# Kernel tuning notes

Measured on AMD Instinct MI355X. Metric: run time of the kernel, lower is better.

## Reference

```python
import jax, jax.numpy as jnp
import numpy as np

B, N, D, H = 8, 128, 768, 64
NEG = -1e30
SLOPE = 0.01  # LeakyReLU slope
EPS = 1e-5    # BatchNorm eps


def setup_inputs() -> dict:
    key = jax.random.key(0)
    ks = jax.random.split(key, 10)
    s = 0.02
    feature = jax.random.normal(ks[0], (B, N, D), jnp.float32)
    aspect = jax.random.normal(ks[1], (B, D), jnp.float32)
    adj = jax.random.randint(ks[2], (B, N, N), 0, 2).astype(jnp.int32)
    W0 = jax.random.normal(ks[3], (D, D), jnp.float32) * s
    b0 = jnp.zeros((D,), jnp.float32)
    W1 = jax.random.normal(ks[4], (D, D), jnp.float32) * s
    b1 = jnp.zeros((D,), jnp.float32)
    A1 = jax.random.normal(ks[5], (2 * D, H), jnp.float32) * s  # afcs[0]
    ab1 = jnp.zeros((H,), jnp.float32)
    A2 = jax.random.normal(ks[6], (H, 1), jnp.float32) * s      # afcs[2]
    ab2 = jnp.zeros((1,), jnp.float32)
    gamma = jnp.ones((D,), jnp.float32)
    beta = jnp.zeros((D,), jnp.float32)
    return dict(feature=feature, aspect=aspect, adj=adj, W0=W0, b0=b0,
                W1=W1, b1=b1, A1=A1, ab1=ab1, A2=A2, ab2=ab2,
                gamma=gamma, beta=beta)


def reference(feature, aspect, adj, W0, b0, W1, b1, A1, ab1, A2, ab2, gamma, beta):
    # aspect is unused by the original forward.
    m = adj.astype(feature.dtype)          # [B,N,N] 0/1 mask
    d = A1.shape[0] // 2
    A1s, A1t = A1[:d], A1[d:]              # weight-split of Linear(2*mem_dim, H):
                                           # [h_i, h_j] @ A1 == h_i @ A1s + h_j @ A1t
    for (W, b) in ((W0, b0), (W1, b1)):
        h = feature @ W + b                # [B,N,D]
        s_src = h @ A1s                    # [B,N,H], broadcast over j
        s_tgt = h @ A1t                    # [B,N,H], broadcast over i
        hid = jax.nn.relu(s_src[:, :, None, :] + s_tgt[:, None, :, :] + ab1)  # [B,N,N,H]
        e = (hid @ A2)[..., 0] + ab2[0]    # [B,N,N]
        e = jnp.where(e > 0, e, SLOPE * e)  # LeakyReLU(0.01)
        logits = e * m + (1.0 - m) * NEG    # mask_logits
        b_, n_ = logits.shape[0], logits.shape[1]
        # NOTE: original softmaxes over the FLATTENED N*N axis, not per-row.
        attn = jax.nn.softmax(logits.reshape(b_, n_ * n_), axis=-1).reshape(b_, n_, n_)
        feature = jnp.einsum('bij,bjd->bid', attn, h)  # attention.bmm(h)
        # dropout is identity in eval / deterministic reference
    node_feature = feature
    g = node_feature.sum(axis=1)           # [B,D]
    mean = g.mean(axis=0)
    var = g.var(axis=0)                    # biased, matches BN training forward
    graph_feature = gamma * (g - mean) / jnp.sqrt(var + EPS) + beta
    return graph_feature, node_feature
```

## Files before the change

kernel.cpp:

```cpp
#include <hip/hip_runtime.h>
#include <math.h>

#define NEG_V (-1e30f)
#define SLOPE_V 0.01f
#define EPS_V 1e-5f

typedef __attribute__((ext_vector_type(8))) short bs8;
typedef __attribute__((ext_vector_type(4))) float f32x4;

__device__ __forceinline__ void split2(float x, unsigned short& hi, unsigned short& lo) {
    unsigned u = __float_as_uint(x);
    unsigned h = (u + 0x7FFFu + ((u >> 16) & 1u)) >> 16;
    hi = (unsigned short)h;
    float hf = __uint_as_float(h << 16);
    float l = x - hf;
    unsigned ul = __float_as_uint(l);
    lo = (unsigned short)((ul + 0x7FFFu + ((ul >> 16) & 1u)) >> 16);
}

__device__ __forceinline__ void mfma_loop(
    const unsigned short* __restrict__ Ahg, const unsigned short* __restrict__ Alg,
    int lda,
    const unsigned short* __restrict__ Bhg, const unsigned short* __restrict__ Blg,
    int ldb, int K, int row0, int col0,
    f32x4 (&acc)[2][2],
    unsigned short (*buf)[64][40])
{
    const int tid = threadIdx.x;
    const int lane = tid & 63, wid = tid >> 6;
    const int wm0 = (wid >> 1) * 32, wn0 = (wid & 1) * 32;
    const int lm = lane & 15, q = lane >> 4;
    const int sr = tid >> 2, sc = (tid & 3) * 8;

    const unsigned short* pAh = Ahg + (size_t)(row0 + sr) * lda + sc;
    const unsigned short* pAl = Alg + (size_t)(row0 + sr) * lda + sc;
    const unsigned short* pBh = Bhg + (size_t)(col0 + sr) * ldb + sc;
    const unsigned short* pBl = Blg + (size_t)(col0 + sr) * ldb + sc;

    bs8 rAh = *(const bs8*)(pAh);
    bs8 rAl = *(const bs8*)(pAl);
    bs8 rBh = *(const bs8*)(pBh);
    bs8 rBl = *(const bs8*)(pBl);

    int st = 0;
    for (int k0 = 0; k0 < K; k0 += 32) {
        unsigned short (*Ah)[40] = buf[st * 4 + 0];
        unsigned short (*Al)[40] = buf[st * 4 + 1];
        unsigned short (*Bh)[40] = buf[st * 4 + 2];
        unsigned short (*Bl)[40] = buf[st * 4 + 3];
        *(bs8*)&Ah[sr][sc] = rAh;
        *(bs8*)&Al[sr][sc] = rAl;
        *(bs8*)&Bh[sr][sc] = rBh;
        *(bs8*)&Bl[sr][sc] = rBl;
        __syncthreads();
        if (k0 + 32 < K) {
            rAh = *(const bs8*)(pAh + k0 + 32);
            rAl = *(const bs8*)(pAl + k0 + 32);
            rBh = *(const bs8*)(pBh + k0 + 32);
            rBl = *(const bs8*)(pBl + k0 + 32);
        }
        bs8 a_h[2], a_l[2], b_h[2], b_l[2];
#pragma unroll
        for (int t = 0; t < 2; t++) {
            a_h[t] = *(bs8*)&Ah[wm0 + t * 16 + lm][q * 8];
            a_l[t] = *(bs8*)&Al[wm0 + t * 16 + lm][q * 8];
            b_h[t] = *(bs8*)&Bh[wn0 + t * 16 + lm][q * 8];
            b_l[t] = *(bs8*)&Bl[wn0 + t * 16 + lm][q * 8];
        }
#pragma unroll
        for (int mt = 0; mt < 2; mt++)
#pragma unroll
            for (int nt = 0; nt < 2; nt++) {
                acc[mt][nt] = __builtin_amdgcn_mfma_f32_16x16x32_bf16(a_h[mt], b_h[nt], acc[mt][nt], 0, 0, 0);
                acc[mt][nt] = __builtin_amdgcn_mfma_f32_16x16x32_bf16(a_h[mt], b_l[nt], acc[mt][nt], 0, 0, 0);
                acc[mt][nt] = __builtin_amdgcn_mfma_f32_16x16x32_bf16(a_l[mt], b_h[nt], acc[mt][nt], 0, 0, 0);
            }
        st ^= 1;
    }
}

__device__ __forceinline__ void transpose_split_tile(
    const float* __restrict__ src, int src_ld,
    unsigned short* __restrict__ dh, unsigned short* __restrict__ dl, int dst_ld,
    unsigned short (*Th)[72], unsigned short (*Tl)[72])
{
    int tid = threadIdx.x;
    int r = tid >> 2;
    int cb = (tid & 3) * 16;
#pragma unroll
    for (int cc = 0; cc < 16; cc += 4) {
        float4 v = *(const float4*)(src + (size_t)r * src_ld + cb + cc);
        unsigned short hh, ll;
        split2(v.x, hh, ll); Th[cb + cc + 0][r] = hh; Tl[cb + cc + 0][r] = ll;
        split2(v.y, hh, ll); Th[cb + cc + 1][r] = hh; Tl[cb + cc + 1][r] = ll;
        split2(v.z, hh, ll); Th[cb + cc + 2][r] = hh; Tl[cb + cc + 2][r] = ll;
        split2(v.w, hh, ll); Th[cb + cc + 3][r] = hh; Tl[cb + cc + 3][r] = ll;
    }
    __syncthreads();
    int n = tid >> 2, ch = (tid & 3) * 8;
    *(bs8*)(dh + (size_t)n * dst_ld + ch)      = *(bs8*)&Th[n][ch];
    *(bs8*)(dh + (size_t)n * dst_ld + ch + 32) = *(bs8*)&Th[n][ch + 32];
    *(bs8*)(dl + (size_t)n * dst_ld + ch)      = *(bs8*)&Tl[n][ch];
    *(bs8*)(dl + (size_t)n * dst_ld + ch + 32) = *(bs8*)&Tl[n][ch + 32];
}

__device__ __forceinline__ void flat_split_job(
    const float* __restrict__ src, unsigned short* __restrict__ dh,
    unsigned short* __restrict__ dl, size_t base)
{
    unsigned short hh, ll;
#pragma unroll
    for (int g = 0; g < 2; g++) {
        bs8 sh, sl;
#pragma unroll
        for (int cc = 0; cc < 8; cc += 4) {
            float4 v = *(const float4*)(src + base + g * 8 + cc);
            split2(v.x, hh, ll); sh[cc + 0] = (short)hh; sl[cc + 0] = (short)ll;
            split2(v.y, hh, ll); sh[cc + 1] = (short)hh; sl[cc + 1] = (short)ll;
            split2(v.z, hh, ll); sh[cc + 2] = (short)hh; sl[cc + 2] = (short)ll;
            split2(v.w, hh, ll); sh[cc + 3] = (short)hh; sl[cc + 3] = (short)ll;
        }
        *(bs8*)(dh + base + g * 8) = sh;
        *(bs8*)(dl + base + g * 8) = sl;
    }
}

__global__ __launch_bounds__(256) void prep_k(
    const float* __restrict__ W0, const float* __restrict__ W1,
    const float* __restrict__ A1, const float* __restrict__ feature,
    const float* __restrict__ b0, const float* __restrict__ b1,
    unsigned short* Wt0h, unsigned short* Wt0l,
    unsigned short* Wt1h, unsigned short* Wt1l,
    unsigned short* fh, unsigned short* fl,
    unsigned short* WAth, unsigned short* WAtl,
    float* bA)
{
    __shared__ __align__(16) char smem[20480];
    int id = blockIdx.x, tid = threadIdx.x;
    if (id < 288) {
        unsigned short (*Th)[72] = (unsigned short(*)[72])(smem);
        unsigned short (*Tl)[72] = (unsigned short(*)[72])(smem + 9216);
        if (id < 144) {
            int kt = id / 12, nt = id % 12;
            transpose_split_tile(W0 + (size_t)(kt * 64) * 768 + nt * 64, 768,
                                 Wt0h + (size_t)(nt * 64) * 768 + kt * 64,
                                 Wt0l + (size_t)(nt * 64) * 768 + kt * 64, 768, Th, Tl);
        } else {
            int r = id - 144, kt = r / 12, nt = r % 12;
            transpose_split_tile(W1 + (size_t)(kt * 64) * 768 + nt * 64, 768,
                                 Wt1h + (size_t)(nt * 64) * 768 + kt * 64,
                                 Wt1l + (size_t)(nt * 64) * 768 + kt * 64, 768, Th, Tl);
        }
    } else if (id < 480) {
        flat_split_job(feature, fh, fl, (size_t)(id - 288) * 4096 + tid * 16);
    } else if (id < 528) {
        int j = id - 480;
        int rt = j % 12, ct = (j / 12) & 1, layer = j / 24;
        const float* W = layer ? W1 : W0;
        const int r0 = rt * 64;
        unsigned short (*Ah)[40] = (unsigned short(*)[40])(smem);
        unsigned short (*Al)[40] = (unsigned short(*)[40])(smem + 5120);
        unsigned short (*Bh)[40] = (unsigned short(*)[40])(smem + 10240);
        unsigned short (*Bl)[40] = (unsigned short(*)[40])(smem + 15360);
        const int lane = tid & 63, wid = tid >> 6;
        const int wm0 = (wid >> 1) * 32, wn0 = (wid & 1) * 32;
        const int lm = lane & 15, q = lane >> 4;
        const int akk = tid & 31, acs = (tid >> 5) * 8;
        const int br = tid >> 2, bks = (tid & 3) * 8;
        f32x4 acc[2][2] = {};
        for (int k0 = 0; k0 < 768; k0 += 32) {
            {
                const float* ap = A1 + (size_t)(ct * 768 + k0 + akk) * 64 + acs;
                float4 v0 = *(const float4*)ap;
                float4 v1 = *(const float4*)(ap + 4);
                unsigned short hv, lv;
                split2(v0.x, hv, lv); Ah[acs + 0][akk] = hv; Al[acs + 0][akk] = lv;
                split2(v0.y, hv, lv); Ah[acs + 1][akk] = hv; Al[acs + 1][akk] = lv;
                split2(v0.z, hv, lv); Ah[acs + 2][akk] = hv; Al[acs + 2][akk] = lv;
                split2(v0.w, hv, lv); Ah[acs + 3][akk] = hv; Al[acs + 3][akk] = lv;
                split2(v1.x, hv, lv); Ah[acs + 4][akk] = hv; Al[acs + 4][akk] = lv;
                split2(v1.y, hv, lv); Ah[acs + 5][akk] = hv; Al[acs + 5][akk] = lv;
                split2(v1.z, hv, lv); Ah[acs + 6][akk] = hv; Al[acs + 6][akk] = lv;
                split2(v1.w, hv, lv); Ah[acs + 7][akk] = hv; Al[acs + 7][akk] = lv;
            }
            {
                const float* wp = W + (size_t)(r0 + br) * 768 + k0 + bks;
                float4 v0 = *(const float4*)wp;
                float4 v1 = *(const float4*)(wp + 4);
                bs8 sh, sl; unsigned short hv, lv;
                split2(v0.x, hv, lv); sh[0] = (short)hv; sl[0] = (short)lv;
                split2(v0.y, hv, lv); sh[1] = (short)hv; sl[1] = (short)lv;
                split2(v0.z, hv, lv); sh[2] = (short)hv; sl[2] = (short)lv;
                split2(v0.w, hv, lv); sh[3] = (short)hv; sl[3] = (short)lv;
                split2(v1.x, hv, lv); sh[4] = (short)hv; sl[4] = (short)lv;
                split2(v1.y, hv, lv); sh[5] = (short)hv; sl[5] = (short)lv;
                split2(v1.z, hv, lv); sh[6] = (short)hv; sl[6] = (short)lv;
                split2(v1.w, hv, lv); sh[7] = (short)hv; sl[7] = (short)lv;
                *(bs8*)&Bh[br][bks] = sh;
                *(bs8*)&Bl[br][bks] = sl;
            }
            __syncthreads();
            bs8 a_h[2], a_l[2], b_h[2], b_l[2];
#pragma unroll
            for (int t = 0; t < 2; t++) {
                a_h[t] = *(bs8*)&Ah[wm0 + t * 16 + lm][q * 8];
                a_l[t] = *(bs8*)&Al[wm0 + t * 16 + lm][q * 8];
                b_h[t] = *(bs8*)&Bh[wn0 + t * 16 + lm][q * 8];
                b_l[t] = *(bs8*)&Bl[wn0 + t * 16 + lm][q * 8];
            }
#pragma unroll
            for (int mt = 0; mt < 2; mt++)
#pragma unroll
                for (int nt = 0; nt < 2; nt++) {
                    acc[mt][nt] = __builtin_amdgcn_mfma_f32_16x16x32_bf16(a_h[mt], b_h[nt], acc[mt][nt], 0, 0, 0);
                    acc[mt][nt] = __builtin_amdgcn_mfma_f32_16x16x32_bf16(a_h[mt], b_l[nt], acc[mt][nt], 0, 0, 0);
                    acc[mt][nt] = __builtin_amdgcn_mfma_f32_16x16x32_bf16(a_l[mt], b_h[nt], acc[mt][nt], 0, 0, 0);
                }
            __syncthreads();
        }
        const int c0 = ct * 64;
        size_t base = (size_t)layer * 98304;
#pragma unroll
        for (int mt = 0; mt < 2; mt++)
#pragma unroll
            for (int nt = 0; nt < 2; nt++) {
                int n = r0 + wn0 + nt * 16 + lm;
#pragma unroll
                for (int i = 0; i < 4; i++) {
                    int m = c0 + wm0 + mt * 16 + q * 4 + i;
                    unsigned short hv, lv;
                    split2(acc[mt][nt][i], hv, lv);
                    WAth[base + (size_t)m * 768 + n] = hv;
                    WAtl[base + (size_t)m * 768 + n] = lv;
                }
            }
    } else {
        float* redb = (float*)(smem);
        int layer = id - 528;
        const float* bv = layer ? b1 : b0;
        int c = tid & 127, half = tid >> 7;
        float acc = 0.f;
        for (int kk = 0; kk < 384; kk++) {
            int k = half * 384 + kk;
            int row = (c < 64 ? k : 768 + k);
            acc += bv[k] * A1[(size_t)row * 64 + (c & 63)];
        }
        redb[tid] = acc;
        __syncthreads();
        if (tid < 128) bA[layer * 128 + tid] = redb[tid] + redb[tid + 128];
    }
}

__global__ __launch_bounds__(256) void gemm_fused_k(
    const unsigned short* __restrict__ Ahg, const unsigned short* __restrict__ Alg,
    const unsigned short* __restrict__ Wth, const unsigned short* __restrict__ Wtl,
    const unsigned short* __restrict__ WAth, const unsigned short* __restrict__ WAtl,
    const float* __restrict__ bias,
    unsigned short* __restrict__ hth, unsigned short* __restrict__ htl,
    float* __restrict__ s)
{
    __shared__ unsigned short smem[8][64][40];
    int bx = blockIdx.x, row0 = blockIdx.y * 64;
    const unsigned short* Bh;
    const unsigned short* Bl;
    int col0;
    if (bx < 12) { Bh = Wth;  Bl = Wtl;  col0 = bx * 64; }
    else         { Bh = WAth; Bl = WAtl; col0 = (bx - 12) * 64; }
    f32x4 acc[2][2] = {};
    mfma_loop(Ahg, Alg, 768, Bh, Bl, 768, 768, row0, col0, acc, smem);
    int tid = threadIdx.x, lane = tid & 63, wid = tid >> 6;
    int wm0 = (wid >> 1) * 32, wn0 = (wid & 1) * 32;
    int lm = lane & 15, q = lane >> 4;
    if (bx >= 12) {
#pragma unroll
        for (int mt = 0; mt < 2; mt++)
#pragma unroll
            for (int nt = 0; nt < 2; nt++) {
                int c = col0 + wn0 + nt * 16 + lm;
#pragma unroll
                for (int i = 0; i < 4; i++) {
                    int r = row0 + wm0 + mt * 16 + q * 4 + i;
                    s[(size_t)r * 128 + c] = acc[mt][nt][i];
                }
            }
        return;
    }
    __syncthreads();
    unsigned short* flat = &smem[0][0][0];
    unsigned short (*Hi)[69] = (unsigned short(*)[69])flat;
    unsigned short (*Lo)[69] = (unsigned short(*)[69])(flat + 4416);
#pragma unroll
    for (int mt = 0; mt < 2; mt++)
#pragma unroll
        for (int nt = 0; nt < 2; nt++) {
            int c = wn0 + nt * 16 + lm;
            float bv = bias[col0 + c];
#pragma unroll
            for (int i = 0; i < 4; i++) {
                int r = wm0 + mt * 16 + q * 4 + i;
                unsigned short hv, lv;
                split2(acc[mt][nt][i] + bv, hv, lv);
                Hi[r][c] = hv; Lo[r][c] = lv;
            }
        }
    __syncthreads();
    int d = tid >> 2, kq = (tid & 3) * 16;
    int b = row0 >> 7, kb = row0 & 127;
    bs8 th0, th1, tl0, tl1;
#pragma unroll
    for (int e = 0; e < 8; e++) {
        th0[e] = Hi[kq + e][d];     th1[e] = Hi[kq + 8 + e][d];
        tl0[e] = Lo[kq + e][d];     tl1[e] = Lo[kq + 8 + e][d];
    }
    size_t to = ((size_t)b * 768 + col0 + d) * 128 + kb + kq;
    *(bs8*)(hth + to) = th0; *(bs8*)(hth + to + 8) = th1;
    *(bs8*)(htl + to) = tl0; *(bs8*)(htl + to + 8) = tl1;
}

__global__ __launch_bounds__(256) void score_k(
    const float* __restrict__ s, const int* __restrict__ adj,
    const float* __restrict__ ab1, const float* __restrict__ A2,
    const float* __restrict__ ab2, const float* __restrict__ bA,
    unsigned short* __restrict__ ph, unsigned short* __restrict__ pl,
    float* __restrict__ psum)
{
    __shared__ float st[128][65];
    __shared__ float ss[4][65];
    __shared__ float a2s[64];
    __shared__ float warr[4];
    const int bx = blockIdx.x, b = blockIdx.y, tid = threadIdx.x;
    const int i0 = bx * 4;
    for (int idx = tid; idx < 8192; idx += 256) {
        int j = idx >> 6, h2 = idx & 63;
        st[j][h2] = s[(size_t)(b * 128 + j) * 128 + 64 + h2] + bA[64 + h2];
    }
    {
        int i = tid >> 6, h2 = tid & 63;
        ss[i][h2] = s[(size_t)(b * 128 + i0 + i) * 128 + h2] + bA[h2] + ab1[h2];
    }
    if (tid < 64) a2s[tid] = A2[tid];
    __syncthreads();
    const float ab2v = ab2[0];
    const int rr = tid >> 7;
    const int j = tid & 127;
    const int r0 = rr * 2, r1 = rr * 2 + 1;
    float acc0 = 0.f, acc1 = 0.f;
#pragma unroll 4
    for (int h2 = 0; h2 < 64; h2++) {
        float bb = st[j][h2];
        float cv = a2s[h2];
        acc0 = fmaf(fmaxf(ss[r0][h2] + bb, 0.f), cv, acc0);
        acc1 = fmaf(fmaxf(ss[r1][h2] + bb, 0.f), cv, acc1);
    }
    float e0 = acc0 + ab2v; e0 = (e0 > 0.f) ? e0 : SLOPE_V * e0;
    float e1 = acc1 + ab2v; e1 = (e1 > 0.f) ? e1 : SLOPE_V * e1;
    size_t o0 = (size_t)b * 16384 + (size_t)(i0 + r0) * 128 + j;
    size_t o1 = (size_t)b * 16384 + (size_t)(i0 + r1) * 128 + j;
    float v0 = adj[o0] ? expf(e0) : 0.f;
    float v1 = adj[o1] ? expf(e1) : 0.f;
    unsigned short hv, lv;
    split2(v0, hv, lv); ph[o0] = hv; pl[o0] = lv;
    split2(v1, hv, lv); ph[o1] = hv; pl[o1] = lv;
    float vs = v0 + v1;
#pragma unroll
    for (int o = 32; o > 0; o >>= 1) vs += __shfl_down(vs, o);
    if ((tid & 63) == 0) warr[tid >> 6] = vs;
    __syncthreads();
    if (tid == 0) psum[b * 32 + bx] = warr[0] + warr[1] + warr[2] + warr[3];
}

__global__ __launch_bounds__(256) void attn_mfma_k(
    const unsigned short* __restrict__ ph, const unsigned short* __restrict__ pl,
    const unsigned short* __restrict__ hth, const unsigned short* __restrict__ htl,
    const float* __restrict__ psum, float* __restrict__ node,
    unsigned short* __restrict__ nodeh, unsigned short* __restrict__ nodel)
{
    __shared__ unsigned short smem[8][64][40];
    __shared__ float sred[33];
    int b = blockIdx.z;
    int row0 = blockIdx.y * 64, col0 = blockIdx.x * 64;
    int tid = threadIdx.x;
    if (tid < 32) sred[tid] = psum[b * 32 + tid];
    __syncthreads();
    if (tid == 0) {
        float t = 0.f;
#pragma unroll
        for (int i = 0; i < 32; i++) t += sred[i];
        sred[32] = 1.0f / t;
    }
    __syncthreads();
    float alpha = sred[32];
    f32x4 acc[2][2] = {};
    mfma_loop(ph + (size_t)b * 16384, pl + (size_t)b * 16384, 128,
              hth + (size_t)b * 98304, htl + (size_t)b * 98304, 128, 128,
              row0, col0, acc, smem);
    __syncthreads();
    float* C = node + (size_t)b * 98304;
    unsigned short* flat = &smem[0][0][0];
    unsigned short (*Hi)[69] = (unsigned short(*)[69])flat;
    unsigned short (*Lo)[69] = (unsigned short(*)[69])(flat + 4416);
    int lane = tid & 63, wid = tid >> 6;
    int wm0 = (wid >> 1) * 32, wn0 = (wid & 1) * 32;
    int lm = lane & 15, q = lane >> 4;
#pragma unroll
    for (int mt = 0; mt < 2; mt++)
#pragma unroll
        for (int nt = 0; nt < 2; nt++) {
            int c = wn0 + nt * 16 + lm;
#pragma unroll
            for (int i = 0; i < 4; i++) {
                int r = wm0 + mt * 16 + q * 4 + i;
                float v = acc[mt][nt][i] * alpha;
                C[(size_t)(row0 + r) * 768 + col0 + c] = v;
                unsigned short hv, lv;
                split2(v, hv, lv);
                Hi[r][c] = hv; Lo[r][c] = lv;
            }
        }
    __syncthreads();
    int r = tid >> 2, cq = (tid & 3) * 16;
    bs8 vh0, vh1, vl0, vl1;
#pragma unroll
    for (int e = 0; e < 8; e++) {
        vh0[e] = Hi[r][cq + e];     vh1[e] = Hi[r][cq + 8 + e];
        vl0[e] = Lo[r][cq + e];     vl1[e] = Lo[r][cq + 8 + e];
    }
    size_t ro = (size_t)(b * 128 + row0 + r) * 768 + col0 + cq;
    *(bs8*)(nodeh + ro) = vh0; *(bs8*)(nodeh + ro + 8) = vh1;
    *(bs8*)(nodel + ro) = vl0; *(bs8*)(nodel + ro + 8) = vl1;
}

__global__ __launch_bounds__(512) void gsum_bnorm_k(
    const float* __restrict__ node, const float* __restrict__ gamma,
    const float* __restrict__ beta, float* __restrict__ out)
{
    __shared__ float gbuf[8][64];
    __shared__ float mean_s[64], inv_s[64];
    int tid = threadIdx.x;
    int bg = tid >> 6, dl = tid & 63;
    int d = blockIdx.x * 64 + dl;
    float v = 0.f;
    for (int i = 0; i < 128; i++)
        v += node[(size_t)(bg * 128 + i) * 768 + d];
    gbuf[bg][dl] = v;
    __syncthreads();
    if (tid < 64) {
        float m = 0.f;
#pragma unroll
        for (int b = 0; b < 8; b++) m += gbuf[b][tid];
        m *= 0.125f;
        float var = 0.f;
#pragma unroll
        for (int b = 0; b < 8; b++) { float t = gbuf[b][tid] - m; var += t * t; }
        var *= 0.125f;
        mean_s[tid] = m;
        inv_s[tid] = 1.0f / sqrtf(var + EPS_V);
    }
    __syncthreads();
    out[bg * 768 + d] = gamma[d] * (v - mean_s[dl]) * inv_s[dl] + beta[d];
}

extern "C" void kernel_launch(void* const* d_in, const int* in_sizes, int n_in,
                              void* d_out, int out_size, void* d_ws, size_t ws_size,
                              hipStream_t stream)
{
    const float* feature = (const float*)d_in[0];
    const int*   adj     = (const int*)d_in[2];
    const float* W0      = (const float*)d_in[3];
    const float* b0      = (const float*)d_in[4];
    const float* W1      = (const float*)d_in[5];
    const float* b1      = (const float*)d_in[6];
    const float* A1      = (const float*)d_in[7];
    const float* ab1     = (const float*)d_in[8];
    const float* A2      = (const float*)d_in[9];
    const float* ab2     = (const float*)d_in[10];
    const float* gamma   = (const float*)d_in[11];
    const float* beta    = (const float*)d_in[12];

    float* ws    = (float*)d_ws;
    float* s     = ws;
    float* psum  = ws + 131072;
    float* bA    = ws + 131328;
    unsigned short* u = (unsigned short*)(ws + 131584);
    unsigned short* Wt0h = u;
    unsigned short* Wt0l = Wt0h + 589824;
    unsigned short* Wt1h = Wt0l + 589824;
    unsigned short* Wt1l = Wt1h + 589824;
    unsigned short* WAth = Wt1l + 589824;
    unsigned short* WAtl = WAth + 196608;
    unsigned short* fh   = WAtl + 196608;
    unsigned short* fl   = fh + 786432;
    unsigned short* hth  = fl + 786432;
    unsigned short* htl  = hth + 786432;
    unsigned short* ndh  = htl + 786432;
    unsigned short* ndl  = ndh + 786432;
    unsigned short* ph   = ndl + 786432;
    unsigned short* pl   = ph + 131072;

    float* out       = (float*)d_out;
    float* graph_out = out;
    float* node_out  = out + 6144;

    prep_k<<<530, 256, 0, stream>>>(W0, W1, A1, feature, b0, b1,
                                    Wt0h, Wt0l, Wt1h, Wt1l,
                                    fh, fl, WAth, WAtl, bA);

    for (int layer = 0; layer < 2; layer++) {
        const unsigned short* Wth = layer ? Wt1h : Wt0h;
        const unsigned short* Wtl = layer ? Wt1l : Wt0l;
        const float* bb = layer ? b1 : b0;
        const unsigned short* Ahg = layer ? ndh : fh;
        const unsigned short* Alg = layer ? ndl : fl;
        gemm_fused_k<<<dim3(14, 16), 256, 0, stream>>>(
            Ahg, Alg, Wth, Wtl, WAth + (size_t)layer * 98304,
            WAtl + (size_t)layer * 98304, bb, hth, htl, s);
        score_k<<<dim3(32, 8), 256, 0, stream>>>(s, adj, ab1, A2, ab2,
                                                 bA + layer * 128, ph, pl, psum);
        attn_mfma_k<<<dim3(12, 2, 8), 256, 0, stream>>>(ph, pl, hth, htl, psum,
                                                        node_out, ndh, ndl);
    }
    gsum_bnorm_k<<<12, 512, 0, stream>>>(node_out, gamma, beta, graph_out);
}
```

Measured before the change: 175.6 us.

## Deepen global prefetch in GEMM loops and vectorize score/gsum loads

The shared MFMA GEMM loop and the W·A1 prep GEMM now keep two K-slices of global loads in flight by unrolling the loop by two over alternating register sets. This is meant to hide more global load latency behind the MFMA work. Separately, the score kernel's staging of s into shared memory uses float4 loads, and the graph-sum reduction uses four independent accumulators to expose more memory parallelism. The cost is higher register pressure and a K loop that assumes K is a multiple of 64.

```diff
diff --git a/kernel.cpp b/kernel.cpp
--- a/kernel.cpp
+++ b/kernel.cpp
@@ -7,6 +7,7 @@
 
 typedef __attribute__((ext_vector_type(8))) short bs8;
 typedef __attribute__((ext_vector_type(4))) float f32x4;
+
 
 __device__ __forceinline__ void split2(float x, unsigned short& hi, unsigned short& lo) {
     unsigned u = __float_as_uint(x);
@@ -18,6 +19,26 @@
     lo = (unsigned short)((ul + 0x7FFFu + ((ul >> 16) & 1u)) >> 16);
 }
 
+#define MFMA_COMPUTE(B0)                                                       \
+    {                                                                          \
+        bs8 a_h[2], a_l[2], b_h[2], b_l[2];                                    \
+        _Pragma("unroll")                                                      \
+        for (int t = 0; t < 2; t++) {                                          \
+            a_h[t] = *(bs8*)&buf[(B0) + 0][wm0 + t * 16 + lm][q * 8];          \
+            a_l[t] = *(bs8*)&buf[(B0) + 1][wm0 + t * 16 + lm][q * 8];          \
+            b_h[t] = *(bs8*)&buf[(B0) + 2][wn0 + t * 16 + lm][q * 8];          \
+            b_l[t] = *(bs8*)&buf[(B0) + 3][wn0 + t * 16 + lm][q * 8];          \
+        }                                                                      \
+        _Pragma("unroll")                                                      \
+        for (int mt = 0; mt < 2; mt++)                                         \
+            _Pragma("unroll")                                                  \
+            for (int nt = 0; nt < 2; nt++) {                                   \
+                acc[mt][nt] = __builtin_amdgcn_mfma_f32_16x16x32_bf16(a_h[mt], b_h[nt], acc[mt][nt], 0, 0, 0); \
+                acc[mt][nt] = __builtin_amdgcn_mfma_f32_16x16x32_bf16(a_h[mt], b_l[nt], acc[mt][nt], 0, 0, 0); \
+                acc[mt][nt] = __builtin_amdgcn_mfma_f32_16x16x32_bf16(a_l[mt], b_h[nt], acc[mt][nt], 0, 0, 0); \
+            }                                                                  \
+    }
+
 __device__ __forceinline__ void mfma_loop(
     const unsigned short* __restrict__ Ahg, const unsigned short* __restrict__ Alg,
     int lda,
@@ -37,45 +58,40 @@
     const unsigned short* pBh = Bhg + (size_t)(col0 + sr) * ldb + sc;
     const unsigned short* pBl = Blg + (size_t)(col0 + sr) * ldb + sc;
 
-    bs8 rAh = *(const bs8*)(pAh);
-    bs8 rAl = *(const bs8*)(pAl);
-    bs8 rBh = *(const bs8*)(pBh);
-    bs8 rBl = *(const bs8*)(pBl);
-
-    int st = 0;
-    for (int k0 = 0; k0 < K; k0 += 32) {
-        unsigned short (*Ah)[40] = buf[st * 4 + 0];
-        unsigned short (*Al)[40] = buf[st * 4 + 1];
-        unsigned short (*Bh)[40] = buf[st * 4 + 2];
-        unsigned short (*Bl)[40] = buf[st * 4 + 3];
-        *(bs8*)&Ah[sr][sc] = rAh;
-        *(bs8*)&Al[sr][sc] = rAl;
-        *(bs8*)&Bh[sr][sc] = rBh;
-        *(bs8*)&Bl[sr][sc] = rBl;
+    bs8 xAh = *(const bs8*)(pAh);
+    bs8 xAl = *(const bs8*)(pAl);
+    bs8 xBh = *(const bs8*)(pBh);
+    bs8 xBl = *(const bs8*)(pBl);
+    bs8 yAh = *(const bs8*)(pAh + 32);
+    bs8 yAl = *(const bs8*)(pAl + 32);
+    bs8 yBh = *(const bs8*)(pBh + 32);
+    bs8 yBl = *(const bs8*)(pBl + 32);
+
+    for (int k0 = 0; k0 < K; k0 += 64) {
+        *(bs8*)&buf[0][sr][sc] = xAh;
+        *(bs8*)&buf[1][sr][sc] = xAl;
+        *(bs8*)&buf[2][sr][sc] = xBh;
+        *(bs8*)&buf[3][sr][sc] = xBl;
         __syncthreads();
-        if (k0 + 32 < K) {
-            rAh = *(const bs8*)(pAh + k0 + 32);
-            rAl = *(const bs8*)(pAl + k0 + 32);
-            rBh = *(const bs8*)(pBh + k0 + 32);
-            rBl = *(const bs8*)(pBl + k0 + 32);
-        }
-        bs8 a_h[2], a_l[2], b_h[2], b_l[2];
-#pragma unroll
-        for (int t = 0; t < 2; t++) {
-            a_h[t] = *(bs8*)&Ah[wm0 + t * 16 + lm][q * 8];
-            a_l[t] = *(bs8*)&Al[wm0 + t * 16 + lm][q * 8];
-            b_h[t] = *(bs8*)&Bh[wn0 + t * 16 + lm][q * 8];
-            b_l[t] = *(bs8*)&Bl[wn0 + t * 16 + lm][q * 8];
-        }
-#pragma unroll
-        for (int mt = 0; mt < 2; mt++)
-#pragma unroll
-            for (int nt = 0; nt < 2; nt++) {
-                acc[mt][nt] = __builtin_amdgcn_mfma_f32_16x16x32_bf16(a_h[mt], b_h[nt], acc[mt][nt], 0, 0, 0);
-                acc[mt][nt] = __builtin_amdgcn_mfma_f32_16x16x32_bf16(a_h[mt], b_l[nt], acc[mt][nt], 0, 0, 0);
-                acc[mt][nt] = __builtin_amdgcn_mfma_f32_16x16x32_bf16(a_l[mt], b_h[nt], acc[mt][nt], 0, 0, 0);
-            }
-        st ^= 1;
+        if (k0 + 64 < K) {
+            xAh = *(const bs8*)(pAh + k0 + 64);
+            xAl = *(const bs8*)(pAl + k0 + 64);
+            xBh = *(const bs8*)(pBh + k0 + 64);
+            xBl = *(const bs8*)(pBl + k0 + 64);
+        }
+        MFMA_COMPUTE(0);
+        *(bs8*)&buf[4][sr][sc] = yAh;
+        *(bs8*)&buf[5][sr][sc] = yAl;
+        *(bs8*)&buf[6][sr][sc] = yBh;
+        *(bs8*)&buf[7][sr][sc] = yBl;
+        __syncthreads();
+        if (k0 + 96 < K) {
+            yAh = *(const bs8*)(pAh + k0 + 96);
+            yAl = *(const bs8*)(pAl + k0 + 96);
+            yBh = *(const bs8*)(pBh + k0 + 96);
+            yBl = *(const bs8*)(pBl + k0 + 96);
+        }
+        MFMA_COMPUTE(4);
     }
 }
 
@@ -123,6 +139,48 @@
         *(bs8*)(dh + base + g * 8) = sh;
         *(bs8*)(dl + base + g * 8) = sl;
     }
+}
+
+#define WA_STORE(va0, va1, vw0, vw1) {                                       \
+    unsigned short hv, lv;                                                   \
+    split2((va0).x, hv, lv); Ah[acs + 0][akk] = hv; Al[acs + 0][akk] = lv;   \
+    split2((va0).y, hv, lv); Ah[acs + 1][akk] = hv; Al[acs + 1][akk] = lv;   \
+    split2((va0).z, hv, lv); Ah[acs + 2][akk] = hv; Al[acs + 2][akk] = lv;   \
+    split2((va0).w, hv, lv); Ah[acs + 3][akk] = hv; Al[acs + 3][akk] = lv;   \
+    split2((va1).x, hv, lv); Ah[acs + 4][akk] = hv; Al[acs + 4][akk] = lv;   \
+    split2((va1).y, hv, lv); Ah[acs + 5][akk] = hv; Al[acs + 5][akk] = lv;   \
+    split2((va1).z, hv, lv); Ah[acs + 6][akk] = hv; Al[acs + 6][akk] = lv;   \
+    split2((va1).w, hv, lv); Ah[acs + 7][akk] = hv; Al[acs + 7][akk] = lv;   \
+    bs8 sh, sl;                                                              \
+    split2((vw0).x, hv, lv); sh[0] = (short)hv; sl[0] = (short)lv;           \
+    split2((vw0).y, hv, lv); sh[1] = (short)hv; sl[1] = (short)lv;           \
+    split2((vw0).z, hv, lv); sh[2] = (short)hv; sl[2] = (short)lv;           \
+    split2((vw0).w, hv, lv); sh[3] = (short)hv; sl[3] = (short)lv;           \
+    split2((vw1).x, hv, lv); sh[4] = (short)hv; sl[4] = (short)lv;           \
+    split2((vw1).y, hv, lv); sh[5] = (short)hv; sl[5] = (short)lv;           \
+    split2((vw1).z, hv, lv); sh[6] = (short)hv; sl[6] = (short)lv;           \
+    split2((vw1).w, hv, lv); sh[7] = (short)hv; sl[7] = (short)lv;           \
+    *(bs8*)&Bh[br][bks] = sh;                                                \
+    *(bs8*)&Bl[br][bks] = sl;                                                \
+}
+
+#define WA_FRAG() {                                                          \
+    bs8 a_h[2], a_l[2], b_h[2], b_l[2];                                      \
+    _Pragma("unroll")                                                        \
+    for (int t = 0; t < 2; t++) {                                            \
+        a_h[t] = *(bs8*)&Ah[wm0 + t * 16 + lm][q * 8];                       \
+        a_l[t] = *(bs8*)&Al[wm0 + t * 16 + lm][q * 8];                       \
+        b_h[t] = *(bs8*)&Bh[wn0 + t * 16 + lm][q * 8];                       \
+        b_l[t] = *(bs8*)&Bl[wn0 + t * 16 + lm][q * 8];                       \
+    }                                                                        \
+    _Pragma("unroll")                                                        \
+    for (int mt = 0; mt < 2; mt++)                                           \
+        _Pragma("unroll")                                                    \
+        for (int nt = 0; nt < 2; nt++) {                                     \
+            acc[mt][nt] = __builtin_amdgcn_mfma_f32_16x16x32_bf16(a_h[mt], b_h[nt], acc[mt][nt], 0, 0, 0); \
+            acc[mt][nt] = __builtin_amdgcn_mfma_f32_16x16x32_bf16(a_h[mt], b_l[nt], acc[mt][nt], 0, 0, 0); \
+            acc[mt][nt] = __builtin_amdgcn_mfma_f32_16x16x32_bf16(a_l[mt], b_h[nt], acc[mt][nt], 0, 0, 0); \
+        }                                                                    \
 }
 
 __global__ __launch_bounds__(256) void prep_k(
@@ -167,55 +225,37 @@
         const int lm = lane & 15, q = lane >> 4;
         const int akk = tid & 31, acs = (tid >> 5) * 8;
         const int br = tid >> 2, bks = (tid & 3) * 8;
+        const float* A1p = A1 + (size_t)(ct * 768 + akk) * 64 + acs;
+        const float* Wp  = W + (size_t)(r0 + br) * 768 + bks;
+        float4 xa0 = *(const float4*)(A1p);
+        float4 xa1 = *(const float4*)(A1p + 4);
+        float4 xw0 = *(const float4*)(Wp);
+        float4 xw1 = *(const float4*)(Wp + 4);
+        float4 ya0 = *(const float4*)(A1p + 32 * 64);
+        float4 ya1 = *(const float4*)(A1p + 32 * 64 + 4);
+        float4 yw0 = *(const float4*)(Wp + 32);
+        float4 yw1 = *(const float4*)(Wp + 36);
         f32x4 acc[2][2] = {};
-        for (int k0 = 0; k0 < 768; k0 += 32) {
-            {
-                const float* ap = A1 + (size_t)(ct * 768 + k0 + akk) * 64 + acs;
-                float4 v0 = *(const float4*)ap;
-                float4 v1 = *(const float4*)(ap + 4);
-                unsigned short hv, lv;
-                split2(v0.x, hv, lv); Ah[acs + 0][akk] = hv; Al[acs + 0][akk] = lv;
-                split2(v0.y, hv, lv); Ah[acs + 1][akk] = hv; Al[acs + 1][akk] = lv;
-                split2(v0.z, hv, lv); Ah[acs + 2][akk] = hv; Al[acs + 2][akk] = lv;
-                split2(v0.w, hv, lv); Ah[acs + 3][akk] = hv; Al[acs + 3][akk] = lv;
-                split2(v1.x, hv, lv); Ah[acs + 4][akk] = hv; Al[acs + 4][akk] = lv;
-                split2(v1.y, hv, lv); Ah[acs + 5][akk] = hv; Al[acs + 5][akk] = lv;
-                split2(v1.z, hv, lv); Ah[acs + 6][akk] = hv; Al[acs + 6][akk] = lv;
-                split2(v1.w, hv, lv); Ah[acs + 7][akk] = hv; Al[acs + 7][akk] = lv;
+        for (int k0 = 0; k0 < 768; k0 += 64) {
+            WA_STORE(xa0, xa1, xw0, xw1);
+            __syncthreads();
+            if (k0 + 64 < 768) {
+                xa0 = *(const float4*)(A1p + (size_t)(k0 + 64) * 64);
+                xa1 = *(const float4*)(A1p + (size_t)(k0 + 64) * 64 + 4);
+                xw0 = *(const float4*)(Wp + k0 + 64);
+                xw1 = *(const float4*)(Wp + k0 + 68);
             }
-            {
-                const float* wp = W + (size_t)(r0 + br) * 768 + k0 + bks;
-                float4 v0 = *(const float4*)wp;
-                float4 v1 = *(const float4*)(wp + 4);
-                bs8 sh, sl; unsigned short hv, lv;
-                split2(v0.x, hv, lv); sh[0] = (short)hv; sl[0] = (short)lv;
-                split2(v0.y, hv, lv); sh[1] = (short)hv; sl[1] = (short)lv;
-                split2(v0.z, hv, lv); sh[2] = (short)hv; sl[2] = (short)lv;
-                split2(v0.w, hv, lv); sh[3] = (short)hv; sl[3] = (short)lv;
-                split2(v1.x, hv, lv); sh[4] = (short)hv; sl[4] = (short)lv;
-                split2(v1.y, hv, lv); sh[5] = (short)hv; sl[5] = (short)lv;
-                split2(v1.z, hv, lv); sh[6] = (short)hv; sl[6] = (short)lv;
-                split2(v1.w, hv, lv); sh[7] = (short)hv; sl[7] = (short)lv;
-                *(bs8*)&Bh[br][bks] = sh;
-                *(bs8*)&Bl[br][bks] = sl;
+            WA_FRAG();
+            __syncthreads();
+            WA_STORE(ya0, ya1, yw0, yw1);
+            __syncthreads();
+            if (k0 + 96 < 768) {
+                ya0 = *(const float4*)(A1p + (size_t)(k0 + 96) * 64);
+                ya1 = *(const float4*)(A1p + (size_t)(k0 + 96) * 64 + 4);
+                yw0 = *(const float4*)(Wp + k0 + 96);
+                yw1 = *(const float4*)(Wp + k0 + 100);
             }
-            __syncthreads();
-            bs8 a_h[2], a_l[2], b_h[2], b_l[2];
-#pragma unroll
-            for (int t = 0; t < 2; t++) {
-                a_h[t] = *(bs8*)&Ah[wm0 + t * 16 + lm][q * 8];
-                a_l[t] = *(bs8*)&Al[wm0 + t * 16 + lm][q * 8];
-                b_h[t] = *(bs8*)&Bh[wn0 + t * 16 + lm][q * 8];
-                b_l[t] = *(bs8*)&Bl[wn0 + t * 16 + lm][q * 8];
-            }
-#pragma unroll
-            for (int mt = 0; mt < 2; mt++)
-#pragma unroll
-                for (int nt = 0; nt < 2; nt++) {
-                    acc[mt][nt] = __builtin_amdgcn_mfma_f32_16x16x32_bf16(a_h[mt], b_h[nt], acc[mt][nt], 0, 0, 0);
-                    acc[mt][nt] = __builtin_amdgcn_mfma_f32_16x16x32_bf16(a_h[mt], b_l[nt], acc[mt][nt], 0, 0, 0);
-                    acc[mt][nt] = __builtin_amdgcn_mfma_f32_16x16x32_bf16(a_l[mt], b_h[nt], acc[mt][nt], 0, 0, 0);
-                }
+            WA_FRAG();
             __syncthreads();
         }
         const int c0 = ct * 64;
@@ -330,9 +370,17 @@
     __shared__ float warr[4];
     const int bx = blockIdx.x, b = blockIdx.y, tid = threadIdx.x;
     const int i0 = bx * 4;
-    for (int idx = tid; idx < 8192; idx += 256) {
-        int j = idx >> 6, h2 = idx & 63;
-        st[j][h2] = s[(size_t)(b * 128 + j) * 128 + 64 + h2] + bA[64 + h2];
+#pragma unroll
+    for (int g = 0; g < 8; g++) {
+        int idx4 = tid + g * 256;
+        int j = idx4 >> 4;
+        int h2 = (idx4 & 15) * 4;
+        float4 v = *(const float4*)&s[(size_t)(b * 128 + j) * 128 + 64 + h2];
+        float4 bv = *(const float4*)&bA[64 + h2];
+        st[j][h2 + 0] = v.x + bv.x;
+        st[j][h2 + 1] = v.y + bv.y;
+        st[j][h2 + 2] = v.z + bv.z;
+        st[j][h2 + 3] = v.w + bv.w;
     }
     {
         int i = tid >> 6, h2 = tid & 63;
@@ -439,9 +487,16 @@
     int tid = threadIdx.x;
     int bg = tid >> 6, dl = tid & 63;
     int d = blockIdx.x * 64 + dl;
-    float v = 0.f;
-    for (int i = 0; i < 128; i++)
-        v += node[(size_t)(bg * 128 + i) * 768 + d];
+    const float* np = node + (size_t)(bg * 128) * 768 + d;
+    float a0 = 0.f, a1 = 0.f, a2 = 0.f, a3 = 0.f;
+#pragma unroll 4
+    for (int i = 0; i < 128; i += 4) {
+        a0 += np[(size_t)(i + 0) * 768];
+        a1 += np[(size_t)(i + 1) * 768];
+        a2 += np[(size_t)(i + 2) * 768];
+        a3 += np[(size_t)(i + 3) * 768];
+    }
+    float v = (a0 + a1) + (a2 + a3);
     gbuf[bg][dl] = v;
     __syncthreads();
     if (tid < 64) {
```

Result: faster. 161.6 us (-8.0%).
